# Performance work log

Measured on AMD Instinct MI355X. Metric: run time of the kernel, lower is better.

## Reference

```python
import jax, jax.numpy as jnp
import numpy as np

NBIT = 8


def _qmm(x, W, key):
    """Bit-serial quantized matmul with per-bit noisy weights (faithful to torch quantization()).
    x: (..., in), W: (out, in). Returns z (..., out), min, max, last noisy weight."""
    nsplit = 2 ** NBIT - 1
    mn = jnp.min(x)
    mx = jnp.max(x)
    q = ((x - mn) / (mx - mn) * nsplit).astype(jnp.uint8)  # trunc cast like torch .type(uint8)
    z = jnp.zeros(x.shape[:-1] + (W.shape[0],), x.dtype)
    Wn = W
    for i in range(NBIT):  # fixed 8-bit loop
        noise = jax.random.normal(jax.random.fold_in(key, i), W.shape, W.dtype) * jnp.abs(W) * 0.1
        Wn = W + noise
        bit = ((q >> i) & 1).astype(x.dtype) * float(2 ** i)
        z = z + jnp.matmul(bit, Wn.T)
    return z, mn, mx, Wn  # Wn = weight left in fc after loop (last bit's noisy weight)


def _requant(z, mn, mx, W_last):
    nsplit = 2 ** NBIT - 1
    bias = jnp.sum(mn * W_last, axis=1)  # (out,)
    return z / nsplit * (mx - mn) + bias


def _bn(x2d, gamma, beta, eps=1e-5):
    m = x2d.mean(axis=0)
    v = x2d.var(axis=0)  # biased, like torch BN training normalization
    return (x2d - m) / jnp.sqrt(v + eps) * gamma + beta


def _forward(node_embedding, edge_embedding, nbr_mask, c_two, c_two2, c_three, c_three2,
             bn2_g, bn2_b, bn3_g, bn3_b, nbr_idx):
    B, At, Nbr, Fe = edge_embedding.shape
    Fn = node_embedding.shape[-1]
    gather = jax.vmap(lambda x, i: x[i])  # batched fancy gather along atom axis
    key = jax.random.key(42)

    # two-body
    node_i = jnp.broadcast_to(node_embedding[:, :, None, :], (B, At, Nbr, Fn))
    node_j = gather(node_embedding, nbr_idx) * nbr_mask[..., None]  # (B,At,Nbr,Fn)
    c2 = jnp.concatenate([node_i, node_j], axis=3)  # (B,At,Nbr,2Fn)
    z, mn, mx, Wl = _qmm(c2, c_two, jax.random.fold_in(key, 0))
    c2 = jax.nn.relu(_requant(z, mn, mx, Wl))
    z, mn, mx, Wl = _qmm(c2, c_two2, jax.random.fold_in(key, 1))
    c2 = _requant(z, mn, mx, Wl)
    g2, e2 = jnp.split(c2, 2, axis=3)
    two = jax.nn.sigmoid(g2) * jnp.tanh(e2)
    two = _bn(two.reshape(-1, Fe), bn2_g, bn2_b).reshape(B, At, Nbr, Fe)

    # three-body
    nbr_jk = gather(nbr_idx, nbr_idx)                 # (B,At,Nbr,Nbr) neighbors-of-neighbors
    node_k = gather(node_embedding, nbr_jk)           # (B,At,Nbr,Nbr,Fn)
    edge_jk = gather(edge_embedding, nbr_idx)         # (B,At,Nbr,Nbr,Fe)
    edge_ij = jnp.broadcast_to(edge_embedding[:, :, :, None, :], (B, At, Nbr, Nbr, Fe))
    c3 = jnp.concatenate([
        jnp.broadcast_to(node_i[:, :, :, None, :], (B, At, Nbr, Nbr, Fn)),
        jnp.broadcast_to(node_j[:, :, :, None, :], (B, At, Nbr, Nbr, Fn)),
        node_k, edge_ij, edge_jk], axis=4)            # (B,At,Nbr,Nbr,3Fn+2Fe)
    z, mn, mx, Wl = _qmm(c3, c_three, jax.random.fold_in(key, 2))
    c3 = jax.nn.relu(_requant(z, mn, mx, Wl))
    z, mn, mx, Wl = _qmm(c3, c_three2, jax.random.fold_in(key, 3))
    c3 = _requant(z, mn, mx, Wl)
    g3, e3 = jnp.split(c3, 2, axis=4)
    three = jax.nn.sigmoid(g3) * jnp.tanh(e3)
    mask_jk = gather(nbr_mask, nbr_idx)               # (B,At,Nbr,Nbr) = nbr_mask[b, nbr_idx[b,i,j], k]
    three = (three * mask_jk[..., None]).sum(axis=3)  # (B,At,Nbr,Fe)
    three = _bn(three.reshape(-1, Fe), bn3_g, bn3_b).reshape(B, At, Nbr, Fe)

    return jax.nn.relu(edge_embedding + two + three)


def setup_inputs() -> dict:
    key = jax.random.key(0)
    ks = jax.random.split(key, 8)
    B, At, Nbr, Fn, Fe = 4, 48, 20, 64, 64
    return {
        "node_embedding": jax.random.normal(ks[0], (B, At, Fn), jnp.float32),
        "edge_embedding": jax.random.normal(ks[1], (B, At, Nbr, Fe), jnp.float32),
        "nbr_mask": jnp.ones((B, At, Nbr), jnp.float32),
        "c_two": jax.random.normal(ks[2], (8 * Fn, 2 * Fn), jnp.float32) * 0.05,
        "c_two2": jax.random.normal(ks[3], (2 * Fe, 8 * Fn), jnp.float32) * 0.05,
        "c_three": jax.random.normal(ks[4], (6 * Fn + 4 * Fe, 3 * Fn + 2 * Fe), jnp.float32) * 0.05,
        "c_three2": jax.random.normal(ks[5], (2 * Fe, 6 * Fn + 4 * Fe), jnp.float32) * 0.05,
        "bn2_g": jnp.ones((Fe,), jnp.float32),
        "bn2_b": jnp.zeros((Fe,), jnp.float32),
        "bn3_g": jnp.ones((Fe,), jnp.float32),
        "bn3_b": jnp.zeros((Fe,), jnp.float32),
        "nbr_idx": jax.random.randint(ks[6], (B, At, Nbr), 0, At, jnp.int32),
    }


def reference(node_embedding, edge_embedding, nbr_mask, c_two, c_two2, c_three, c_three2,
              bn2_g, bn2_b, bn3_g, bn3_b, nbr_idx):
    return _forward(node_embedding, edge_embedding, nbr_mask, c_two, c_two2, c_three, c_three2,
                    bn2_g, bn2_b, bn3_g, bn3_b, nbr_idx)
```

## Files before the change

kernel.cpp:

```cpp
#include <hip/hip_runtime.h>
#include <cstdint>
#include <cstddef>

#define DEVI __device__ __forceinline__

typedef __attribute__((ext_vector_type(8))) short s8v;
typedef __attribute__((ext_vector_type(4))) float f4v;

static constexpr int B_ = 4, AT = 48, NBRS = 20;
static constexpr int R2 = B_ * AT * NBRS;
static constexpr int M4 = R2 * NBRS;

static constexpr size_t OFF_B2A  = 0;
static constexpr size_t OFF_B2B  = OFF_B2A + 524288;
static constexpr size_t OFF_B3A  = OFF_B2B + 524288;
static constexpr size_t OFF_BW3B = OFF_B3A + 1638400;
static constexpr size_t OFF_BN3B = OFF_BW3B + 81920;
static constexpr size_t OFF_W72A = OFF_BN3B + 327680;
static constexpr size_t OFF_W72B = OFF_W72A + 65536;
static constexpr size_t OFF_W73A = OFF_W72B + 65536;
static constexpr size_t OFF_W73B = OFF_W73A + 204800;
static constexpr size_t OFF_RS   = OFF_W73B + 81920;
static constexpr size_t OFF_SLOT = OFF_RS + 1408;
static constexpr size_t OFF_BN   = OFF_SLOT + 16;
static constexpr size_t OFF_C2IN = OFF_BN + 256;
static constexpr size_t OFF_Z1   = OFF_C2IN + (size_t)R2 * 128;
static constexpr size_t OFF_C2B  = OFF_Z1 + (size_t)R2 * 512;
static constexpr size_t OFF_Z2   = OFF_C2B + (size_t)R2 * 512;
static constexpr size_t OFF_TWO  = OFF_Z2 + (size_t)R2 * 128;
static constexpr size_t OFF_NK   = OFF_TWO + (size_t)R2 * 64;
static constexpr size_t OFF_P2   = OFF_NK + (size_t)R2 * 64;
static constexpr size_t OFF_P3   = OFF_P2 + (size_t)R2 * 640;
static constexpr size_t OFF_TSUM = OFF_P3 + (size_t)R2 * 640;
static constexpr size_t OFF_Q2A  = OFF_TSUM + (size_t)R2 * 64;
static constexpr size_t OFF_Q2B  = OFF_Q2A + 122880;
static constexpr size_t OFF_QP2  = OFF_Q2B + 491520;
static constexpr size_t OFF_QP3  = OFF_QP2 + 184320;

DEVI void tf2x32(unsigned k0, unsigned k1, unsigned x0, unsigned x1,
                 unsigned& o0, unsigned& o1) {
  unsigned ks0 = k0, ks1 = k1, ks2 = k0 ^ k1 ^ 0x1BD11BDAu;
  x0 += ks0; x1 += ks1;
  const unsigned rotA[4] = {13u, 15u, 26u, 6u};
  const unsigned rotB[4] = {17u, 29u, 16u, 24u};
  unsigned ks[3] = {ks0, ks1, ks2};
  #pragma unroll
  for (int i = 0; i < 5; ++i) {
    const unsigned* rot = (i & 1) ? rotB : rotA;
    #pragma unroll
    for (int r = 0; r < 4; ++r) {
      x0 += x1;
      x1 = (x1 << rot[r]) | (x1 >> (32u - rot[r]));
      x1 ^= x0;
    }
    x0 += ks[(i + 1) % 3];
    x1 += ks[(i + 2) % 3] + (unsigned)(i + 1);
  }
  o0 = x0; o1 = x1;
}

DEVI float erfinv_xla(float x) {
  float w = -log1pf(-x * x);
  float p;
  if (w < 5.f) {
    w -= 2.5f;
    p = 2.81022636e-08f;
    p = fmaf(p, w, 3.43273939e-07f);
    p = fmaf(p, w, -3.5233877e-06f);
    p = fmaf(p, w, -4.39150654e-06f);
    p = fmaf(p, w, 0.00021858087f);
    p = fmaf(p, w, -0.00125372503f);
    p = fmaf(p, w, -0.00417768164f);
    p = fmaf(p, w, 0.246640727f);
    p = fmaf(p, w, 1.50140941f);
  } else {
    w = sqrtf(w) - 3.f;
    p = -0.000200214257f;
    p = fmaf(p, w, 0.000100950558f);
    p = fmaf(p, w, 0.00134934322f);
    p = fmaf(p, w, -0.00367342844f);
    p = fmaf(p, w, 0.00573950773f);
    p = fmaf(p, w, -0.0076224613f);
    p = fmaf(p, w, 0.00943887047f);
    p = fmaf(p, w, 1.00167406f);
    p = fmaf(p, w, 2.83297682f);
  }
  return p * x;
}

DEVI float normal_from_bits(unsigned bits) {
  unsigned fb = (bits >> 9) | 0x3F800000u;
  float f = __uint_as_float(fb) - 1.0f;
  const float lo = -0.99999994f;
  float u = f * (1.0f - lo) + lo;
  u = fmaxf(lo, u);
  return 1.41421356237f * erfinv_xla(u);
}

DEVI unsigned f2o(float f) { unsigned u = __float_as_uint(f); return (u & 0x80000000u) ? ~u : (u | 0x80000000u); }
DEVI float o2f(unsigned u) { return (u & 0x80000000u) ? __uint_as_float(u & 0x7FFFFFFFu) : __uint_as_float(~u); }

DEVI unsigned short f2bf(float x) {
  unsigned u = __float_as_uint(x);
  return (unsigned short)((u + 0x7FFFu + ((u >> 16) & 1u)) >> 16);
}
DEVI float bf2f(unsigned short h) { return __uint_as_float((unsigned)h << 16); }

DEVI void blockMinMax(float lmn, float lmx, float* smem, unsigned* slot) {
  float* smn = smem; float* smx = smem + 256;
  int t = threadIdx.x;
  smn[t] = lmn; smx[t] = lmx;
  __syncthreads();
  for (int s = 128; s > 0; s >>= 1) {
    if (t < s) { smn[t] = fminf(smn[t], smn[t + s]); smx[t] = fmaxf(smx[t], smx[t + s]); }
    __syncthreads();
  }
  if (t == 0) { atomicMin(slot + 0, f2o(smn[0])); atomicMax(slot + 1, f2o(smx[0])); }
}

DEVI s8v expand_mul(unsigned b) {
  unsigned sl = (b & 15u) * 0x00204081u;
  unsigned sh = ((b >> 4) & 15u) * 0x00204081u;
  union { unsigned u[4]; s8v s; } r;
  r.u[0] = (sl & 0x00010001u) * 0x3F80u;
  r.u[1] = ((sl >> 8) & 0x00010001u) * 0x3F80u;
  r.u[2] = (sh & 0x00010001u) * 0x3F80u;
  r.u[3] = ((sh >> 8) & 0x00010001u) * 0x3F80u;
  return r.s;
}
DEVI int bperm(int bit) { return bit ^ ((((bit) ^ (bit >> 1)) & 1) * 3); }

DEVI s8v bytes_to_bf16(unsigned a, unsigned b) {
  union { unsigned u[4]; s8v s; } r;
  float f0 = (float)(a & 255u), f1 = (float)((a >> 8) & 255u);
  float f2 = (float)((a >> 16) & 255u), f3 = (float)(a >> 24);
  r.u[0] = (__float_as_uint(f0) >> 16) | (__float_as_uint(f1) & 0xFFFF0000u);
  r.u[1] = (__float_as_uint(f2) >> 16) | (__float_as_uint(f3) & 0xFFFF0000u);
  f0 = (float)(b & 255u); f1 = (float)((b >> 8) & 255u);
  f2 = (float)((b >> 16) & 255u); f3 = (float)(b >> 24);
  r.u[2] = (__float_as_uint(f0) >> 16) | (__float_as_uint(f1) & 0xFFFF0000u);
  r.u[3] = (__float_as_uint(f2) >> 16) | (__float_as_uint(f3) & 0xFFFF0000u);
  return r.s;
}

__global__ __launch_bounds__(256) void k_prep(
    const float* __restrict__ W2A, const float* __restrict__ W2B,
    const float* __restrict__ W3A, const float* __restrict__ W3B,
    short* __restrict__ B2A, short* __restrict__ B2B, short* __restrict__ B3A,
    short* __restrict__ BW3B, short* __restrict__ BN3B,
    float* __restrict__ W72A, float* __restrict__ W72B,
    float* __restrict__ W73A, float* __restrict__ W73B,
    float* __restrict__ z1, float* __restrict__ z2, float* __restrict__ tsum,
    unsigned* __restrict__ slots) {
  int t = blockIdx.x * 256 + threadIdx.x;
  if (t < R2 * 512) z1[t] = 0.f;
  if (t < R2 * 128) z2[t] = 0.f;
  if (t < R2 * 64) tsum[t] = 0.f;
  if (t < 4) { slots[2 * t] = f2o(3.402823466e38f); slots[2 * t + 1] = f2o(-3.402823466e38f); }
  int lt = t;
  const float* W; float* W7; int N, K; unsigned layer; int which;
  if (lt < 524288) { W = W2A; W7 = W72A; N = 512; K = 128; layer = 0u; which = 0; }
  else if ((lt -= 524288) < 524288) { W = W2B; W7 = W72B; N = 128; K = 512; layer = 1u; which = 1; }
  else if ((lt -= 524288) < 1638400) { W = W3A; W7 = W73A; N = 640; K = 320; layer = 2u; which = 2; }
  else if ((lt -= 1638400) < 655360) { W = W3B; W7 = W73B; N = 128; K = 640; layer = 3u; which = 3; }
  else return;
  int n_elem = N * K;
  int bit = lt / n_elem;
  int e = lt - bit * n_elem;
  unsigned kl0, kl1, kb0, kb1, r0, r1;
  tf2x32(0u, 42u, 0u, layer, kl0, kl1);
  tf2x32(kl0, kl1, 0u, (unsigned)bit, kb0, kb1);
  tf2x32(kb0, kb1, 0u, (unsigned)e, r0, r1);
  float w = W[e];
  float nz = normal_from_bits(r0 ^ r1) * fabsf(w) * 0.1f;
  float wn = w + nz;
  int n = e / K, k = e - n * K;
  if (bit == 7) W7[e] = wn;
  if (which == 3) {
    BN3B[((size_t)(n >> 4) * 160 + (size_t)(k >> 2)) * 512
         + (size_t)((k & 3) * 16 + (n & 15)) * 8 + bperm(bit)] = (short)f2bf(ldexpf(nz, bit));
    if (bit == 0) {
      unsigned short hi = f2bf(w);
      unsigned short lo = f2bf(w - bf2f(hi));
      size_t o2 = (((size_t)(n >> 4) * 20 + (size_t)(k >> 5)) * 2) * 512
                + (size_t)(((k >> 3) & 3) * 16 + (n & 15)) * 8 + (k & 7);
      BW3B[o2] = (short)hi; BW3B[o2 + 512] = (short)lo;
    }
  } else {
    float sv = ldexpf(wn, bit);
    unsigned short hi = f2bf(sv);
    unsigned short lo = f2bf(sv - bf2f(hi));
    int pk = k;
    if (which == 2) {
      if (k >= 128 && k < 192) pk = k + 64;
      else if (k >= 192 && k < 256) pk = k - 64;
    }
    short* Bf = (which == 0) ? B2A : (which == 1 ? B2B : B3A);
    int KG = K >> 2;
    size_t off = (((size_t)(n >> 4) * KG + (size_t)(pk >> 2)) * 2) * 512
               + (size_t)((pk & 3) * 16 + (n & 15)) * 8 + bperm(bit);
    Bf[off] = (short)hi; Bf[off + 512] = (short)lo;
  }
}

__global__ __launch_bounds__(256) void k_build2(
    const float* __restrict__ node, const float* __restrict__ mask,
    const int* __restrict__ nidx, float* __restrict__ c2in, float* __restrict__ NK,
    const float* __restrict__ W72A, const float* __restrict__ W72B,
    const float* __restrict__ W73A, const float* __restrict__ W73B,
    float* __restrict__ rs, unsigned* __restrict__ slot) {
  __shared__ float sred[512];
  int idx = blockIdx.x * 256 + threadIdx.x;
  float lmn = 3.4e38f, lmx = -3.4e38f;
  if (idx < R2 * 128) {
    int row = idx >> 7, c = idx & 127;
    float v;
    if (c < 64) v = node[(size_t)(row / 20) * 64 + c];
    else {
      int b = row / 960;
      v = node[(size_t)(b * 48 + nidx[row]) * 64 + (c - 64)] * mask[row];
    }
    c2in[idx] = v; lmn = v; lmx = v;
  } else if (idx < R2 * 192) {
    int i2 = idx - R2 * 128;
    int row = i2 >> 6, c = i2 & 63;
    int b = row / 960;
    NK[i2] = node[(size_t)(b * 48 + nidx[row]) * 64 + c];
  } else if (idx < R2 * 192 + 1408) {
    int o = idx - R2 * 192;
    const float* p; int cols; int dsto;
    if (o < 512) { p = W72A; cols = 128; dsto = o; }
    else if (o < 640) { p = W72B; cols = 512; dsto = o; o -= 512; }
    else if (o < 1280) { p = W73A; cols = 320; dsto = o; o -= 640; }
    else { p = W73B; cols = 640; dsto = o; o -= 1280; }
    const float* rowp = p + (size_t)o * cols;
    float s = 0.f;
    for (int j = 0; j < cols; ++j) s += rowp[j];
    rs[dsto] = s;
  }
  blockMinMax(lmn, lmx, sred, slot);
}

__global__ __launch_bounds__(256) void k_qm4(
    const float* __restrict__ node, const float* __restrict__ edge,
    const float* __restrict__ c2in, const float* __restrict__ NK,
    const int* __restrict__ nidx, const unsigned* __restrict__ slot0,
    unsigned char* __restrict__ Q2A, unsigned* __restrict__ slot4) {
  __shared__ float sred[512];
  int idx0 = blockIdx.x * 256 + threadIdx.x;
  if (idx0 < R2 * 128) {
    const float mn = o2f(slot0[0]), mx = o2f(slot0[1]);
    float invd = 255.f / (mx - mn);
    Q2A[idx0] = (unsigned char)((c2in[idx0] - mn) * invd);
  }
  const int n0 = 12288, n1 = n0 + 245760, n2 = n1 + 245760, total = n2 + 4915200;
  float lmn = 3.4e38f, lmx = -3.4e38f;
  for (int idx = idx0; idx < total; idx += gridDim.x * 256) {
    float v, v2;
    if (idx < n0) { v = node[idx]; v2 = v; }
    else if (idx < n1) { v = edge[idx - n0]; v2 = v; }
    else if (idx < n2) {
      int j = idx - n1; int r = j >> 6, c = j & 63;
      v = c2in[(size_t)r * 128 + 64 + c]; v2 = v;
    } else {
      int j = idx - n2; int bij = j / 1280, t = j - bij * 1280;
      int b = bij / 960;
      size_t base = (size_t)((b * 48 + nidx[bij]) * 20) * 64 + t;
      v = NK[base]; v2 = edge[base];
    }
    lmn = fminf(lmn, fminf(v, v2)); lmx = fmaxf(lmx, fmaxf(v, v2));
  }
  blockMinMax(lmn, lmx, sred, slot4);
}

__global__ __launch_bounds__(256) void k_mfma_gemm(
    const unsigned char* __restrict__ Q, int ldq,
    const short* __restrict__ B, int KGfull, int kg0,
    int M, int Nfull, int KB, float* __restrict__ Z, int accflag) {
  const int tid = threadIdx.x;
  const int lane = tid & 63, w = tid >> 6;
  const int l15 = lane & 15, l4 = lane >> 4;
  const int mbase = blockIdx.y * 64;
  const int nbase = blockIdx.x * 128;
  const int kq0 = blockIdx.z * KB;
  f4v acc[4][2];
  #pragma unroll
  for (int a = 0; a < 4; ++a)
    #pragma unroll
    for (int b = 0; b < 2; ++b) acc[a][b] = f4v{0.f, 0.f, 0.f, 0.f};
  for (int ks16 = 0; ks16 < KB; ks16 += 16) {
    uint4 qv[4];
    #pragma unroll
    for (int mf = 0; mf < 4; ++mf)
      qv[mf] = *(const uint4*)(Q + (size_t)(mbase + mf * 16 + l15) * ldq + kq0 + ks16);
    #pragma unroll
    for (int sub = 0; sub < 4; ++sub) {
      int kg = kg0 + ((kq0 + ks16) >> 2) + sub;
      s8v af[4];
      #pragma unroll
      for (int mf = 0; mf < 4; ++mf) {
        unsigned wv = (sub == 0) ? qv[mf].x : (sub == 1) ? qv[mf].y : (sub == 2) ? qv[mf].z : qv[mf].w;
        af[mf] = expand_mul((wv >> (l4 * 8)) & 255u);
      }
      #pragma unroll
      for (int j = 0; j < 2; ++j) {
        size_t o = (((size_t)(nbase / 16 + w * 2 + j) * KGfull + kg) * 2) * 512 + (size_t)lane * 8;
        s8v bh = *(const s8v*)(B + o);
        s8v bl = *(const s8v*)(B + o + 512);
        #pragma unroll
        for (int mf = 0; mf < 4; ++mf) {
          acc[mf][j] = __builtin_amdgcn_mfma_f32_16x16x32_bf16(af[mf], bh, acc[mf][j], 0, 0, 0);
          acc[mf][j] = __builtin_amdgcn_mfma_f32_16x16x32_bf16(af[mf], bl, acc[mf][j], 0, 0, 0);
        }
      }
    }
  }
  #pragma unroll
  for (int mf = 0; mf < 4; ++mf) {
    #pragma unroll
    for (int r = 0; r < 4; ++r) {
      int m = mbase + mf * 16 + l4 * 4 + r;
      float* zp = Z + (size_t)m * Nfull + nbase;
      #pragma unroll
      for (int j = 0; j < 2; ++j) {
        int n = (w * 2 + j) * 16 + l15;
        if (accflag == 0) zp[n] = acc[mf][j][r];
        else atomicAdd(zp + n, acc[mf][j][r]);
      }
    }
  }
}

__global__ __launch_bounds__(256) void k_act1(const float* __restrict__ z1, const float* __restrict__ rs,
                                              const unsigned* __restrict__ slot0,
                                              unsigned* __restrict__ slot1) {
  __shared__ float sred[512];
  const float mn = o2f(slot0[0]), mx = o2f(slot0[1]);
  int idx = blockIdx.x * 256 + threadIdx.x;
  float lmn = 3.4e38f, lmx = -3.4e38f;
  if (idx < R2 * 512) {
    int o = idx & 511;
    float v = fmaxf(0.f, z1[idx] * (1.f / 255.f) * (mx - mn) + mn * rs[o]);
    lmn = v; lmx = v;
  }
  blockMinMax(lmn, lmx, sred, slot1);
}

__global__ __launch_bounds__(256) void k_qq(
    const float* __restrict__ z1, const float* __restrict__ rs,
    const float* __restrict__ node, const float* __restrict__ edge,
    const float* __restrict__ c2in, const float* __restrict__ NK,
    const int* __restrict__ nidx, const unsigned* __restrict__ slot0,
    const unsigned* __restrict__ slot2, const unsigned* __restrict__ slot4,
    unsigned char* __restrict__ Q2B, unsigned char* __restrict__ QP2, unsigned char* __restrict__ QP3) {
  int idx = blockIdx.x * 256 + threadIdx.x;
  if (idx < R2 * 512) {
    const float mn0 = o2f(slot0[0]), mx0 = o2f(slot0[1]);
    const float mn = o2f(slot2[0]), mx = o2f(slot2[1]);
    int o = idx & 511;
    float v = fmaxf(0.f, z1[idx] * (1.f / 255.f) * (mx0 - mn0) + mn0 * rs[o]);
    Q2B[idx] = (unsigned char)((v - mn) * (255.f / (mx - mn)));
    return;
  }
  int j = idx - R2 * 512;
  const int seg = 245760;
  if (j >= 5 * seg) return;
  const float mn = o2f(slot4[0]), mx = o2f(slot4[1]);
  const float invd = 255.f / (mx - mn);
  int s = j / seg; int jj = j - s * seg;
  int r = jj >> 6, c = jj & 63;
  float v; unsigned char* dst;
  if (s == 0)      { v = node[(size_t)(r / 20) * 64 + c];  dst = QP2 + (size_t)r * 192 + c; }
  else if (s == 1) { v = c2in[(size_t)r * 128 + 64 + c];   dst = QP2 + (size_t)r * 192 + 64 + c; }
  else if (s == 2) { v = edge[(size_t)r * 64 + c];         dst = QP2 + (size_t)r * 192 + 128 + c; }
  else if (s == 3) { v = NK[(size_t)r * 64 + c];           dst = QP3 + (size_t)r * 128 + c; }
  else             { v = edge[(size_t)r * 64 + c];         dst = QP3 + (size_t)r * 128 + 64 + c; }
  *dst = (unsigned char)((v - mn) * invd);
}

__global__ __launch_bounds__(256) void k_mfma_p23(
    const unsigned char* __restrict__ Q2, const unsigned char* __restrict__ Q3,
    const short* __restrict__ B, float* __restrict__ P2, float* __restrict__ P3) {
  const int half = blockIdx.y >= 60;
  const int by = blockIdx.y - half * 60;
  const unsigned char* Q = half ? Q3 : Q2;
  float* Z = half ? P3 : P2;
  const int kg0 = half ? 48 : 0;
  const int KB = half ? 128 : 192;
  const int ldq = half ? 128 : 192;
  const int tid = threadIdx.x;
  const int lane = tid & 63, w = tid >> 6;
  const int l15 = lane & 15, l4 = lane >> 4;
  const int mbase = by * 64;
  const int nbase = blockIdx.x * 128;
  f4v acc[4][2];
  #pragma unroll
  for (int a = 0; a < 4; ++a)
    #pragma unroll
    for (int b = 0; b < 2; ++b) acc[a][b] = f4v{0.f, 0.f, 0.f, 0.f};
  for (int ks16 = 0; ks16 < KB; ks16 += 16) {
    uint4 qv[4];
    #pragma unroll
    for (int mf = 0; mf < 4; ++mf)
      qv[mf] = *(const uint4*)(Q + (size_t)(mbase + mf * 16 + l15) * ldq + ks16);
    #pragma unroll
    for (int sub = 0; sub < 4; ++sub) {
      int kg = kg0 + (ks16 >> 2) + sub;
      s8v af[4];
      #pragma unroll
      for (int mf = 0; mf < 4; ++mf) {
        unsigned wv = (sub == 0) ? qv[mf].x : (sub == 1) ? qv[mf].y : (sub == 2) ? qv[mf].z : qv[mf].w;
        af[mf] = expand_mul((wv >> (l4 * 8)) & 255u);
      }
      #pragma unroll
      for (int j = 0; j < 2; ++j) {
        size_t o = (((size_t)(nbase / 16 + w * 2 + j) * 80 + kg) * 2) * 512 + (size_t)lane * 8;
        s8v bh = *(const s8v*)(B + o);
        s8v bl = *(const s8v*)(B + o + 512);
        #pragma unroll
        for (int mf = 0; mf < 4; ++mf) {
          acc[mf][j] = __builtin_amdgcn_mfma_f32_16x16x32_bf16(af[mf], bh, acc[mf][j], 0, 0, 0);
          acc[mf][j] = __builtin_amdgcn_mfma_f32_16x16x32_bf16(af[mf], bl, acc[mf][j], 0, 0, 0);
        }
      }
    }
  }
  #pragma unroll
  for (int mf = 0; mf < 4; ++mf) {
    #pragma unroll
    for (int r = 0; r < 4; ++r) {
      int m = mbase + mf * 16 + l4 * 4 + r;
      float* zp = Z + (size_t)m * 640 + nbase;
      #pragma unroll
      for (int j = 0; j < 2; ++j)
        zp[(w * 2 + j) * 16 + l15] = acc[mf][j][r];
    }
  }
}

__global__ __launch_bounds__(256) void k_act2mm3(
    const float* __restrict__ z2, const float* __restrict__ rs2b,
    const unsigned* __restrict__ slot2, float* __restrict__ two,
    const float* __restrict__ P12, const float* __restrict__ P3,
    const float* __restrict__ rs3a, const int* __restrict__ nidx,
    const unsigned* __restrict__ slot4, unsigned* __restrict__ slot6) {
  __shared__ float p12s[640];
  __shared__ float bias[640];
  __shared__ float sred[512];
  int gid = blockIdx.x * 256 + threadIdx.x;
  if (gid < R2 * 64) {
    const float mn = o2f(slot2[0]), mx = o2f(slot2[1]);
    int row = gid >> 6, c = gid & 63;
    float d = (mx - mn) * (1.f / 255.f);
    float g = z2[(size_t)row * 128 + c] * d + mn * rs2b[c];
    float e = z2[(size_t)row * 128 + 64 + c] * d + mn * rs2b[64 + c];
    two[gid] = (1.f / (1.f + expf(-g))) * tanhf(e);
  }
  const int bij = blockIdx.x;
  const int b = bij / 960;
  const int jp = nidx[bij];
  const size_t p3b = (size_t)((b * 48 + jp) * 20) * 640;
  const float mn2 = o2f(slot4[0]), mx2 = o2f(slot4[1]);
  const float sc2 = (mx2 - mn2) * (1.f / 255.f);
  for (int k = threadIdx.x; k < 640; k += 256) {
    p12s[k] = P12[(size_t)bij * 640 + k];
    bias[k] = mn2 * rs3a[k];
  }
  __syncthreads();
  float lmn = 3.4e38f, lmx = -3.4e38f;
  for (int t = threadIdx.x; t < 20 * 640; t += 256) {
    int knb = t / 640, k = t - knb * 640;
    float v = fmaxf(0.f, (p12s[k] + P3[p3b + t]) * sc2 + bias[k]);
    lmn = fminf(lmn, v); lmx = fmaxf(lmx, v);
  }
  blockMinMax(lmn, lmx, sred, slot6);
}

__global__ __launch_bounds__(256) void k_mfma_l3b(
    const float* __restrict__ P12, const float* __restrict__ P3,
    const float* __restrict__ rs3a, const float* __restrict__ rs3b,
    const short* __restrict__ BW, const short* __restrict__ BN,
    const int* __restrict__ nidx, const float* __restrict__ mask,
    const unsigned* __restrict__ slotA, const unsigned* __restrict__ slotB,
    float* __restrict__ tsum) {
  __shared__ unsigned char qt[64 * 648];
  const int tid = threadIdx.x;
  const int s0 = blockIdx.x * 64;
  const float mn2 = o2f(slotA[0]), mx2 = o2f(slotA[1]);
  const float mn3 = o2f(slotB[0]), mx3 = o2f(slotB[1]);
  const float sc2 = (mx2 - mn2) * (1.f / 255.f);
  const float invd3 = 255.f / (mx3 - mn3);
  {
    int r = tid >> 2, kq = (tid & 3) * 160;
    int s = s0 + r;
    int bij = s / 20, knb = s - bij * 20, b = bij / 960;
    int p3row = (b * 48 + nidx[bij]) * 20 + knb;
    const float* pa = P12 + (size_t)bij * 640;
    const float* pb = P3 + (size_t)p3row * 640;
    for (int k = kq; k < kq + 160; k += 4) {
      float4 va = *(const float4*)(pa + k);
      float4 vb = *(const float4*)(pb + k);
      float4 rv = *(const float4*)(rs3a + k);
      float v0 = fmaxf(0.f, (va.x + vb.x) * sc2 + mn2 * rv.x);
      float v1 = fmaxf(0.f, (va.y + vb.y) * sc2 + mn2 * rv.y);
      float v2 = fmaxf(0.f, (va.z + vb.z) * sc2 + mn2 * rv.z);
      float v3 = fmaxf(0.f, (va.w + vb.w) * sc2 + mn2 * rv.w);
      unsigned pk = (unsigned)((v0 - mn3) * invd3) | ((unsigned)((v1 - mn3) * invd3) << 8)
                  | ((unsigned)((v2 - mn3) * invd3) << 16) | ((unsigned)((v3 - mn3) * invd3) << 24);
      *(unsigned*)(&qt[(size_t)r * 648 + k]) = pk;
    }
  }
  __syncthreads();
  const int lane = tid & 63, w = tid >> 6;
  const int l15 = lane & 15, l4 = lane >> 4;
  const int nf0 = w, nf1 = w + 4;
  const unsigned char* qr[4];
  #pragma unroll
  for (int mf = 0; mf < 4; ++mf) qr[mf] = qt + (size_t)(mf * 16 + l15) * 648;
  const size_t bb0 = (size_t)nf0 * 160 * 512 + (size_t)lane * 8;
  const size_t bb1 = (size_t)nf1 * 160 * 512 + (size_t)lane * 8;
  f4v acc[4][2];
  #pragma unroll
  for (int a = 0; a < 4; ++a)
    #pragma unroll
    for (int b = 0; b < 2; ++b) acc[a][b] = f4v{0.f, 0.f, 0.f, 0.f};
  s8v c00 = *(const s8v*)(BN + bb0), c01 = *(const s8v*)(BN + bb1);
  s8v c10 = *(const s8v*)(BN + bb0 + 512), c11 = *(const s8v*)(BN + bb1 + 512);
  for (int c = 0; c < 20; ++c) {
    s8v bwh0 = *(const s8v*)(BW + (((size_t)nf0 * 20 + c) * 2) * 512 + (size_t)lane * 8);
    s8v bwh1 = *(const s8v*)(BW + (((size_t)nf1 * 20 + c) * 2) * 512 + (size_t)lane * 8);
    #pragma unroll
    for (int s = 0; s < 8; ++s) {
      const int kg = c * 8 + s;
      s8v af[4];
      #pragma unroll
      for (int mf = 0; mf < 4; ++mf) {
        unsigned wv = *(const unsigned*)(qr[mf] + kg * 4);
        af[mf] = expand_mul((wv >> (l4 * 8)) & 255u);
      }
      s8v nx0 = *(const s8v*)(BN + bb0 + (size_t)(kg + 2) * 512);
      s8v nx1 = *(const s8v*)(BN + bb1 + (size_t)(kg + 2) * 512);
      #pragma unroll
      for (int mf = 0; mf < 4; ++mf) {
        acc[mf][0] = __builtin_amdgcn_mfma_f32_16x16x32_bf16(af[mf], c00, acc[mf][0], 0, 0, 0);
        acc[mf][1] = __builtin_amdgcn_mfma_f32_16x16x32_bf16(af[mf], c01, acc[mf][1], 0, 0, 0);
      }
      c00 = c10; c01 = c11; c10 = nx0; c11 = nx1;
    }
    {
      s8v aq[4];
      #pragma unroll
      for (int mf = 0; mf < 4; ++mf) {
        unsigned a0 = *(const unsigned*)(qr[mf] + c * 32 + l4 * 8);
        unsigned a1 = *(const unsigned*)(qr[mf] + c * 32 + l4 * 8 + 4);
        aq[mf] = bytes_to_bf16(a0, a1);
      }
      #pragma unroll
      for (int mf = 0; mf < 4; ++mf) {
        acc[mf][0] = __builtin_amdgcn_mfma_f32_16x16x32_bf16(aq[mf], bwh0, acc[mf][0], 0, 0, 0);
        acc[mf][1] = __builtin_amdgcn_mfma_f32_16x16x32_bf16(aq[mf], bwh1, acc[mf][1], 0, 0, 0);
      }
      s8v bwl0 = *(const s8v*)(BW + ((((size_t)nf0 * 20 + c) * 2) + 1) * 512 + (size_t)lane * 8);
      s8v bwl1 = *(const s8v*)(BW + ((((size_t)nf1 * 20 + c) * 2) + 1) * 512 + (size_t)lane * 8);
      #pragma unroll
      for (int mf = 0; mf < 4; ++mf) {
        acc[mf][0] = __builtin_amdgcn_mfma_f32_16x16x32_bf16(aq[mf], bwl0, acc[mf][0], 0, 0, 0);
        acc[mf][1] = __builtin_amdgcn_mfma_f32_16x16x32_bf16(aq[mf], bwl1, acc[mf][1], 0, 0, 0);
      }
    }
  }
  const float d3 = (mx3 - mn3) * (1.f / 255.f);
  const int col = w * 16 + l15;
  const float rg = mn3 * rs3b[col];
  const float re = mn3 * rs3b[64 + col];
  #pragma unroll
  for (int mf = 0; mf < 4; ++mf) {
    #pragma unroll
    for (int r = 0; r < 4; ++r) {
      int s = s0 + mf * 16 + l4 * 4 + r;
      int bij = s / 20, knb = s - bij * 20, b = bij / 960;
      int p3row = (b * 48 + nidx[bij]) * 20 + knb;
      float mk = mask[p3row];
      float g = acc[mf][0][r] * d3 + rg;
      float e = acc[mf][1][r] * d3 + re;
      float val = (1.f / (1.f + expf(-g))) * tanhf(e) * mk;
      atomicAdd(&tsum[(size_t)bij * 64 + col], val);
    }
  }
}

__global__ __launch_bounds__(256) void k_bnstats2(const float* __restrict__ two, const float* __restrict__ tsum,
                                                  float* __restrict__ bn) {
  __shared__ float ss[512];
  const float* x = blockIdx.y ? tsum : two;
  float* mout = bn + (blockIdx.y ? 128 : 0);
  float* vout = mout + 64;
  int c = blockIdx.x, t = threadIdx.x;
  float s = 0.f, q = 0.f;
  for (int r = t; r < R2; r += 256) { float v = x[(size_t)r * 64 + c]; s += v; q += v * v; }
  ss[t] = s; ss[256 + t] = q;
  __syncthreads();
  for (int st = 128; st > 0; st >>= 1) {
    if (t < st) { ss[t] += ss[t + st]; ss[256 + t] += ss[256 + t + st]; }
    __syncthreads();
  }
  if (t == 0) { float m = ss[0] / (float)R2; mout[c] = m; vout[c] = ss[256] / (float)R2 - m * m; }
}

__global__ __launch_bounds__(256) void k_final(const float* __restrict__ edge, const float* __restrict__ two,
                                               const float* __restrict__ tsum, const float* __restrict__ bn,
                                               const float* __restrict__ g2, const float* __restrict__ b2,
                                               const float* __restrict__ g3, const float* __restrict__ b3,
                                               float* __restrict__ out) {
  int idx = blockIdx.x * 256 + threadIdx.x;
  if (idx >= R2 * 64) return;
  int c = idx & 63;
  float t2 = (two[idx] - bn[c]) / sqrtf(bn[64 + c] + 1e-5f) * g2[c] + b2[c];
  float t3 = (tsum[idx] - bn[128 + c]) / sqrtf(bn[192 + c] + 1e-5f) * g3[c] + b3[c];
  out[idx] = fmaxf(0.f, edge[idx] + t2 + t3);
}

extern "C" void kernel_launch(void* const* d_in, const int* in_sizes, int n_in,
                              void* d_out, int out_size, void* d_ws, size_t ws_size,
                              hipStream_t stream) {
  (void)in_sizes; (void)n_in; (void)out_size; (void)ws_size;
  const float* node   = (const float*)d_in[0];
  const float* edge   = (const float*)d_in[1];
  const float* mask   = (const float*)d_in[2];
  const float* c_two  = (const float*)d_in[3];
  const float* c_two2 = (const float*)d_in[4];
  const float* c_three  = (const float*)d_in[5];
  const float* c_three2 = (const float*)d_in[6];
  const float* bn2g = (const float*)d_in[7];
  const float* bn2b = (const float*)d_in[8];
  const float* bn3g = (const float*)d_in[9];
  const float* bn3b = (const float*)d_in[10];
  const int*   nidx = (const int*)d_in[11];
  float* ws = (float*)d_ws;
  unsigned* slots = (unsigned*)(ws + OFF_SLOT);
  float* out = (float*)d_out;
  short* B2A  = (short*)(ws + OFF_B2A);
  short* B2B  = (short*)(ws + OFF_B2B);
  short* B3A  = (short*)(ws + OFF_B3A);
  short* BW3B = (short*)(ws + OFF_BW3B);
  short* BN3B = (short*)(ws + OFF_BN3B);
  unsigned char* Q2A = (unsigned char*)(ws + OFF_Q2A);
  unsigned char* Q2B = (unsigned char*)(ws + OFF_Q2B);
  unsigned char* QP2 = (unsigned char*)(ws + OFF_QP2);
  unsigned char* QP3 = (unsigned char*)(ws + OFF_QP3);
  float* RS = ws + OFF_RS;

  k_prep<<<13056, 256, 0, stream>>>(c_two, c_two2, c_three, c_three2,
                                    B2A, B2B, B3A, BW3B, BN3B,
                                    ws + OFF_W72A, ws + OFF_W72B, ws + OFF_W73A, ws + OFF_W73B,
                                    ws + OFF_Z1, ws + OFF_Z2, ws + OFF_TSUM, slots);
  k_build2<<<2886, 256, 0, stream>>>(node, mask, nidx, ws + OFF_C2IN, ws + OFF_NK,
                                     ws + OFF_W72A, ws + OFF_W72B, ws + OFF_W73A, ws + OFF_W73B,
                                     RS, slots + 0);
  k_qm4<<<2048, 256, 0, stream>>>(node, edge, ws + OFF_C2IN, ws + OFF_NK, nidx, slots + 0,
                                  Q2A, slots + 4);
  k_mfma_gemm<<<dim3(4, 60, 2), 256, 0, stream>>>(Q2A, 128, B2A, 32, 0, 3840, 512, 64, ws + OFF_Z1, 3);
  k_act1<<<7680, 256, 0, stream>>>(ws + OFF_Z1, RS, slots + 0, slots + 2);
  k_qq<<<12480, 256, 0, stream>>>(ws + OFF_Z1, RS, node, edge, ws + OFF_C2IN, ws + OFF_NK,
                                  nidx, slots + 0, slots + 2, slots + 4, Q2B, QP2, QP3);
  k_mfma_gemm<<<dim3(1, 60, 4), 256, 0, stream>>>(Q2B, 512, B2B, 128, 0, 3840, 128, 128, ws + OFF_Z2, 3);
  k_mfma_p23<<<dim3(5, 120), 256, 0, stream>>>(QP2, QP3, B3A, ws + OFF_P2, ws + OFF_P3);
  k_act2mm3<<<3840, 256, 0, stream>>>(ws + OFF_Z2, RS + 512, slots + 2, ws + OFF_TWO,
                                      ws + OFF_P2, ws + OFF_P3, RS + 640, nidx, slots + 4, slots + 6);
  k_mfma_l3b<<<1200, 256, 0, stream>>>(ws + OFF_P2, ws + OFF_P3, RS + 640, RS + 1280,
                                       BW3B, BN3B, nidx, mask, slots + 4, slots + 6, ws + OFF_TSUM);
  k_bnstats2<<<dim3(64, 2), 256, 0, stream>>>(ws + OFF_TWO, ws + OFF_TSUM, ws + OFF_BN);
  k_final<<<960, 256, 0, stream>>>(edge, ws + OFF_TWO, ws + OFF_TSUM, ws + OFF_BN,
                                   bn2g, bn2b, bn3g, bn3b, out);
}
```

Measured before the change: 832.9 us.

## Split K across waves in l3b MFMA kernel with LDS cross-wave reduction

```diff
diff --git a/kernel.cpp b/kernel.cpp
--- a/kernel.cpp
+++ b/kernel.cpp
@@ -476,7 +476,7 @@
   blockMinMax(lmn, lmx, sred, slot6);
 }
 
-__global__ __launch_bounds__(256) void k_mfma_l3b(
+__global__ __launch_bounds__(256, 2) void k_mfma_l3b(
     const float* __restrict__ P12, const float* __restrict__ P3,
     const float* __restrict__ rs3a, const float* __restrict__ rs3b,
     const short* __restrict__ BW, const short* __restrict__ BN,
@@ -513,78 +513,88 @@
   __syncthreads();
   const int lane = tid & 63, w = tid >> 6;
   const int l15 = lane & 15, l4 = lane >> 4;
-  const int nf0 = w, nf1 = w + 4;
   const unsigned char* qr[4];
   #pragma unroll
   for (int mf = 0; mf < 4; ++mf) qr[mf] = qt + (size_t)(mf * 16 + l15) * 648;
-  const size_t bb0 = (size_t)nf0 * 160 * 512 + (size_t)lane * 8;
-  const size_t bb1 = (size_t)nf1 * 160 * 512 + (size_t)lane * 8;
-  f4v acc[4][2];
+  f4v acc[4][8];
   #pragma unroll
   for (int a = 0; a < 4; ++a)
     #pragma unroll
-    for (int b = 0; b < 2; ++b) acc[a][b] = f4v{0.f, 0.f, 0.f, 0.f};
-  s8v c00 = *(const s8v*)(BN + bb0), c01 = *(const s8v*)(BN + bb1);
-  s8v c10 = *(const s8v*)(BN + bb0 + 512), c11 = *(const s8v*)(BN + bb1 + 512);
-  for (int c = 0; c < 20; ++c) {
-    s8v bwh0 = *(const s8v*)(BW + (((size_t)nf0 * 20 + c) * 2) * 512 + (size_t)lane * 8);
-    s8v bwh1 = *(const s8v*)(BW + (((size_t)nf1 * 20 + c) * 2) * 512 + (size_t)lane * 8);
-    #pragma unroll
-    for (int s = 0; s < 8; ++s) {
-      const int kg = c * 8 + s;
-      s8v af[4];
+    for (int b = 0; b < 8; ++b) acc[a][b] = f4v{0.f, 0.f, 0.f, 0.f};
+  const int kg0 = w * 40;
+  s8v cur[8];
+  #pragma unroll
+  for (int j = 0; j < 8; ++j)
+    cur[j] = *(const s8v*)(BN + ((size_t)j * 160 + kg0) * 512 + (size_t)lane * 8);
+  for (int kgl = 0; kgl < 40; ++kgl) {
+    const int kg = kg0 + kgl;
+    s8v af[4];
+    #pragma unroll
+    for (int mf = 0; mf < 4; ++mf) {
+      unsigned wv = *(const unsigned*)(qr[mf] + kg * 4);
+      af[mf] = expand_mul((wv >> (l4 * 8)) & 255u);
+    }
+    s8v nxt[8];
+    #pragma unroll
+    for (int j = 0; j < 8; ++j)
+      nxt[j] = *(const s8v*)(BN + ((size_t)j * 160 + kg + 1) * 512 + (size_t)lane * 8);
+    #pragma unroll
+    for (int j = 0; j < 8; ++j) {
+      #pragma unroll
+      for (int mf = 0; mf < 4; ++mf)
+        acc[mf][j] = __builtin_amdgcn_mfma_f32_16x16x32_bf16(af[mf], cur[j], acc[mf][j], 0, 0, 0);
+    }
+    #pragma unroll
+    for (int j = 0; j < 8; ++j) cur[j] = nxt[j];
+  }
+  #pragma unroll
+  for (int cl = 0; cl < 5; ++cl) {
+    const int c = w * 5 + cl;
+    s8v aq[4];
+    #pragma unroll
+    for (int mf = 0; mf < 4; ++mf) {
+      unsigned a0 = *(const unsigned*)(qr[mf] + c * 32 + l4 * 8);
+      unsigned a1 = *(const unsigned*)(qr[mf] + c * 32 + l4 * 8 + 4);
+      aq[mf] = bytes_to_bf16(a0, a1);
+    }
+    #pragma unroll
+    for (int j = 0; j < 8; ++j) {
+      s8v bh = *(const s8v*)(BW + (((size_t)j * 20 + c) * 2) * 512 + (size_t)lane * 8);
+      s8v bl = *(const s8v*)(BW + (((size_t)j * 20 + c) * 2 + 1) * 512 + (size_t)lane * 8);
       #pragma unroll
       for (int mf = 0; mf < 4; ++mf) {
-        unsigned wv = *(const unsigned*)(qr[mf] + kg * 4);
-        af[mf] = expand_mul((wv >> (l4 * 8)) & 255u);
+        acc[mf][j] = __builtin_amdgcn_mfma_f32_16x16x32_bf16(aq[mf], bh, acc[mf][j], 0, 0, 0);
+        acc[mf][j] = __builtin_amdgcn_mfma_f32_16x16x32_bf16(aq[mf], bl, acc[mf][j], 0, 0, 0);
       }
-      s8v nx0 = *(const s8v*)(BN + bb0 + (size_t)(kg + 2) * 512);
-      s8v nx1 = *(const s8v*)(BN + bb1 + (size_t)(kg + 2) * 512);
-      #pragma unroll
-      for (int mf = 0; mf < 4; ++mf) {
-        acc[mf][0] = __builtin_amdgcn_mfma_f32_16x16x32_bf16(af[mf], c00, acc[mf][0], 0, 0, 0);
-        acc[mf][1] = __builtin_amdgcn_mfma_f32_16x16x32_bf16(af[mf], c01, acc[mf][1], 0, 0, 0);
-      }
-      c00 = c10; c01 = c11; c10 = nx0; c11 = nx1;
-    }
-    {
-      s8v aq[4];
-      #pragma unroll
-      for (int mf = 0; mf < 4; ++mf) {
-        unsigned a0 = *(const unsigned*)(qr[mf] + c * 32 + l4 * 8);
-        unsigned a1 = *(const unsigned*)(qr[mf] + c * 32 + l4 * 8 + 4);
-        aq[mf] = bytes_to_bf16(a0, a1);
-      }
-      #pragma unroll
-      for (int mf = 0; mf < 4; ++mf) {
-        acc[mf][0] = __builtin_amdgcn_mfma_f32_16x16x32_bf16(aq[mf], bwh0, acc[mf][0], 0, 0, 0);
-        acc[mf][1] = __builtin_amdgcn_mfma_f32_16x16x32_bf16(aq[mf], bwh1, acc[mf][1], 0, 0, 0);
-      }
-      s8v bwl0 = *(const s8v*)(BW + ((((size_t)nf0 * 20 + c) * 2) + 1) * 512 + (size_t)lane * 8);
-      s8v bwl1 = *(const s8v*)(BW + ((((size_t)nf1 * 20 + c) * 2) + 1) * 512 + (size_t)lane * 8);
-      #pragma unroll
-      for (int mf = 0; mf < 4; ++mf) {
-        acc[mf][0] = __builtin_amdgcn_mfma_f32_16x16x32_bf16(aq[mf], bwl0, acc[mf][0], 0, 0, 0);
-        acc[mf][1] = __builtin_amdgcn_mfma_f32_16x16x32_bf16(aq[mf], bwl1, acc[mf][1], 0, 0, 0);
-      }
-    }
-  }
+    }
+  }
+  float* zz = (float*)qt;
   const float d3 = (mx3 - mn3) * (1.f / 255.f);
-  const int col = w * 16 + l15;
-  const float rg = mn3 * rs3b[col];
-  const float re = mn3 * rs3b[64 + col];
-  #pragma unroll
   for (int mf = 0; mf < 4; ++mf) {
-    #pragma unroll
-    for (int r = 0; r < 4; ++r) {
-      int s = s0 + mf * 16 + l4 * 4 + r;
+    __syncthreads();
+    #pragma unroll
+    for (int j = 0; j < 8; ++j) {
+      #pragma unroll
+      for (int r = 0; r < 4; ++r)
+        zz[((size_t)w * 16 + l4 * 4 + r) * 132 + j * 16 + l15] = acc[mf][j][r];
+    }
+    __syncthreads();
+    #pragma unroll
+    for (int k = 0; k < 4; ++k) {
+      int o = tid + k * 256;
+      int row = o >> 6, cc = o & 63;
+      float zg = zz[(size_t)row * 132 + cc] + zz[(size_t)(16 + row) * 132 + cc]
+               + zz[(size_t)(32 + row) * 132 + cc] + zz[(size_t)(48 + row) * 132 + cc];
+      float ze = zz[(size_t)row * 132 + 64 + cc] + zz[(size_t)(16 + row) * 132 + 64 + cc]
+               + zz[(size_t)(32 + row) * 132 + 64 + cc] + zz[(size_t)(48 + row) * 132 + 64 + cc];
+      int s = s0 + mf * 16 + row;
       int bij = s / 20, knb = s - bij * 20, b = bij / 960;
       int p3row = (b * 48 + nidx[bij]) * 20 + knb;
       float mk = mask[p3row];
-      float g = acc[mf][0][r] * d3 + rg;
-      float e = acc[mf][1][r] * d3 + re;
+      float g = zg * d3 + mn3 * rs3b[cc];
+      float e = ze * d3 + mn3 * rs3b[64 + cc];
       float val = (1.f / (1.f + expf(-g))) * tanhf(e) * mk;
-      atomicAdd(&tsum[(size_t)bij * 64 + col], val);
+      atomicAdd(&tsum[(size_t)bij * 64 + cc], val);
     }
   }
 }
```

New measurement: 915.7 us. +9.9%, slower.

## Loop bits per thread in weight prep; retile l3b waves to 2x2 fragment grid

Applied to the files above, without the earlier changes.

```diff
diff --git a/kernel.cpp b/kernel.cpp
--- a/kernel.cpp
+++ b/kernel.cpp
@@ -128,7 +128,7 @@
   r.u[3] = ((sh >> 8) & 0x00010001u) * 0x3F80u;
   return r.s;
 }
-DEVI int bperm(int bit) { return bit ^ ((((bit) ^ (bit >> 1)) & 1) * 3); }
+DEVI constexpr int bperm(int bit) { return bit ^ ((((bit) ^ (bit >> 1)) & 1) * 3); }
 
 DEVI s8v bytes_to_bf16(unsigned a, unsigned b) {
   union { unsigned u[4]; s8v s; } r;
@@ -159,37 +159,45 @@
   if (t < 4) { slots[2 * t] = f2o(3.402823466e38f); slots[2 * t + 1] = f2o(-3.402823466e38f); }
   int lt = t;
   const float* W; float* W7; int N, K; unsigned layer; int which;
-  if (lt < 524288) { W = W2A; W7 = W72A; N = 512; K = 128; layer = 0u; which = 0; }
-  else if ((lt -= 524288) < 524288) { W = W2B; W7 = W72B; N = 128; K = 512; layer = 1u; which = 1; }
-  else if ((lt -= 524288) < 1638400) { W = W3A; W7 = W73A; N = 640; K = 320; layer = 2u; which = 2; }
-  else if ((lt -= 1638400) < 655360) { W = W3B; W7 = W73B; N = 128; K = 640; layer = 3u; which = 3; }
+  if (lt < 65536) { W = W2A; W7 = W72A; N = 512; K = 128; layer = 0u; which = 0; }
+  else if ((lt -= 65536) < 65536) { W = W2B; W7 = W72B; N = 128; K = 512; layer = 1u; which = 1; }
+  else if ((lt -= 65536) < 204800) { W = W3A; W7 = W73A; N = 640; K = 320; layer = 2u; which = 2; }
+  else if ((lt -= 204800) < 81920) { W = W3B; W7 = W73B; N = 128; K = 640; layer = 3u; which = 3; }
   else return;
-  int n_elem = N * K;
-  int bit = lt / n_elem;
-  int e = lt - bit * n_elem;
-  unsigned kl0, kl1, kb0, kb1, r0, r1;
+  int e = lt;
+  int n = e / K, k = e - n * K;
+  float w = W[e];
+  float aw = fabsf(w) * 0.1f;
+  unsigned kl0, kl1;
   tf2x32(0u, 42u, 0u, layer, kl0, kl1);
-  tf2x32(kl0, kl1, 0u, (unsigned)bit, kb0, kb1);
-  tf2x32(kb0, kb1, 0u, (unsigned)e, r0, r1);
-  float w = W[e];
-  float nz = normal_from_bits(r0 ^ r1) * fabsf(w) * 0.1f;
-  float wn = w + nz;
-  int n = e / K, k = e - n * K;
-  if (bit == 7) W7[e] = wn;
+  union { short s[8]; s8v v; } hv, lv, bnv;
+  #pragma unroll
+  for (int bit = 0; bit < 8; ++bit) {
+    unsigned kb0, kb1, r0, r1;
+    tf2x32(kl0, kl1, 0u, (unsigned)bit, kb0, kb1);
+    tf2x32(kb0, kb1, 0u, (unsigned)e, r0, r1);
+    float nz = normal_from_bits(r0 ^ r1) * aw;
+    float wn = w + nz;
+    if (bit == 7) W7[e] = wn;
+    if (which == 3) {
+      bnv.s[bperm(bit)] = (short)f2bf(ldexpf(nz, bit));
+    } else {
+      float sv = ldexpf(wn, bit);
+      unsigned short hi = f2bf(sv);
+      unsigned short lo = f2bf(sv - bf2f(hi));
+      hv.s[bperm(bit)] = (short)hi;
+      lv.s[bperm(bit)] = (short)lo;
+    }
+  }
   if (which == 3) {
-    BN3B[((size_t)(n >> 4) * 160 + (size_t)(k >> 2)) * 512
-         + (size_t)((k & 3) * 16 + (n & 15)) * 8 + bperm(bit)] = (short)f2bf(ldexpf(nz, bit));
-    if (bit == 0) {
-      unsigned short hi = f2bf(w);
-      unsigned short lo = f2bf(w - bf2f(hi));
-      size_t o2 = (((size_t)(n >> 4) * 20 + (size_t)(k >> 5)) * 2) * 512
-                + (size_t)(((k >> 3) & 3) * 16 + (n & 15)) * 8 + (k & 7);
-      BW3B[o2] = (short)hi; BW3B[o2 + 512] = (short)lo;
-    }
+    *(s8v*)(BN3B + ((size_t)(n >> 4) * 160 + (size_t)(k >> 2)) * 512
+                 + (size_t)((k & 3) * 16 + (n & 15)) * 8) = bnv.v;
+    unsigned short hi = f2bf(w);
+    unsigned short lo = f2bf(w - bf2f(hi));
+    size_t o2 = (((size_t)(n >> 4) * 20 + (size_t)(k >> 5)) * 2) * 512
+              + (size_t)(((k >> 3) & 3) * 16 + (n & 15)) * 8 + (k & 7);
+    BW3B[o2] = (short)hi; BW3B[o2 + 512] = (short)lo;
   } else {
-    float sv = ldexpf(wn, bit);
-    unsigned short hi = f2bf(sv);
-    unsigned short lo = f2bf(sv - bf2f(hi));
     int pk = k;
     if (which == 2) {
       if (k >= 128 && k < 192) pk = k + 64;
@@ -198,8 +206,9 @@
     short* Bf = (which == 0) ? B2A : (which == 1 ? B2B : B3A);
     int KG = K >> 2;
     size_t off = (((size_t)(n >> 4) * KG + (size_t)(pk >> 2)) * 2) * 512
-               + (size_t)((pk & 3) * 16 + (n & 15)) * 8 + bperm(bit);
-    Bf[off] = (short)hi; Bf[off + 512] = (short)lo;
+               + (size_t)((pk & 3) * 16 + (n & 15)) * 8;
+    *(s8v*)(Bf + off) = hv.v;
+    *(s8v*)(Bf + off + 512) = lv.v;
   }
 }
 
@@ -511,80 +520,95 @@
     }
   }
   __syncthreads();
-  const int lane = tid & 63, w = tid >> 6;
+  const int lane = tid & 63, wave = tid >> 6;
+  const int wm = wave >> 1, wn = wave & 1;
   const int l15 = lane & 15, l4 = lane >> 4;
-  const int nf0 = w, nf1 = w + 4;
-  const unsigned char* qr[4];
-  #pragma unroll
-  for (int mf = 0; mf < 4; ++mf) qr[mf] = qt + (size_t)(mf * 16 + l15) * 648;
-  const size_t bb0 = (size_t)nf0 * 160 * 512 + (size_t)lane * 8;
-  const size_t bb1 = (size_t)nf1 * 160 * 512 + (size_t)lane * 8;
-  f4v acc[4][2];
-  #pragma unroll
-  for (int a = 0; a < 4; ++a)
-    #pragma unroll
-    for (int b = 0; b < 2; ++b) acc[a][b] = f4v{0.f, 0.f, 0.f, 0.f};
-  s8v c00 = *(const s8v*)(BN + bb0), c01 = *(const s8v*)(BN + bb1);
-  s8v c10 = *(const s8v*)(BN + bb0 + 512), c11 = *(const s8v*)(BN + bb1 + 512);
+  const int nfl[4] = {2 * wn, 2 * wn + 1, 2 * wn + 4, 2 * wn + 5};
+  size_t bb[4];
+  #pragma unroll
+  for (int j = 0; j < 4; ++j) bb[j] = ((size_t)nfl[j] * 160) * 512 + (size_t)lane * 8;
+  f4v acc[2][4];
+  #pragma unroll
+  for (int a = 0; a < 2; ++a)
+    #pragma unroll
+    for (int b = 0; b < 4; ++b) acc[a][b] = f4v{0.f, 0.f, 0.f, 0.f};
+  s8v c0[4], c1[4];
+  #pragma unroll
+  for (int j = 0; j < 4; ++j) {
+    c0[j] = *(const s8v*)(BN + bb[j]);
+    c1[j] = *(const s8v*)(BN + bb[j] + 512);
+  }
+  const unsigned char* qrow0 = &qt[(size_t)(wm * 32 + l15) * 648];
+  const unsigned char* qrow1 = qrow0 + 16 * 648;
   for (int c = 0; c < 20; ++c) {
-    s8v bwh0 = *(const s8v*)(BW + (((size_t)nf0 * 20 + c) * 2) * 512 + (size_t)lane * 8);
-    s8v bwh1 = *(const s8v*)(BW + (((size_t)nf1 * 20 + c) * 2) * 512 + (size_t)lane * 8);
+    s8v bwh[4];
+    #pragma unroll
+    for (int j = 0; j < 4; ++j)
+      bwh[j] = *(const s8v*)(BW + (((size_t)nfl[j] * 20 + c) * 2) * 512 + (size_t)lane * 8);
     #pragma unroll
     for (int s = 0; s < 8; ++s) {
       const int kg = c * 8 + s;
-      s8v af[4];
-      #pragma unroll
-      for (int mf = 0; mf < 4; ++mf) {
-        unsigned wv = *(const unsigned*)(qr[mf] + kg * 4);
-        af[mf] = expand_mul((wv >> (l4 * 8)) & 255u);
-      }
-      s8v nx0 = *(const s8v*)(BN + bb0 + (size_t)(kg + 2) * 512);
-      s8v nx1 = *(const s8v*)(BN + bb1 + (size_t)(kg + 2) * 512);
-      #pragma unroll
-      for (int mf = 0; mf < 4; ++mf) {
-        acc[mf][0] = __builtin_amdgcn_mfma_f32_16x16x32_bf16(af[mf], c00, acc[mf][0], 0, 0, 0);
-        acc[mf][1] = __builtin_amdgcn_mfma_f32_16x16x32_bf16(af[mf], c01, acc[mf][1], 0, 0, 0);
-      }
-      c00 = c10; c01 = c11; c10 = nx0; c11 = nx1;
+      unsigned w0 = *(const unsigned*)(qrow0 + kg * 4);
+      unsigned w1 = *(const unsigned*)(qrow1 + kg * 4);
+      s8v af0 = expand_mul((w0 >> (l4 * 8)) & 255u);
+      s8v af1 = expand_mul((w1 >> (l4 * 8)) & 255u);
+      s8v nx[4];
+      #pragma unroll
+      for (int j = 0; j < 4; ++j)
+        nx[j] = *(const s8v*)(BN + bb[j] + (size_t)(kg + 2) * 512);
+      __builtin_amdgcn_s_setprio(1);
+      #pragma unroll
+      for (int j = 0; j < 4; ++j) {
+        acc[0][j] = __builtin_amdgcn_mfma_f32_16x16x32_bf16(af0, c0[j], acc[0][j], 0, 0, 0);
+        acc[1][j] = __builtin_amdgcn_mfma_f32_16x16x32_bf16(af1, c0[j], acc[1][j], 0, 0, 0);
+      }
+      __builtin_amdgcn_s_setprio(0);
+      #pragma unroll
+      for (int j = 0; j < 4; ++j) { c0[j] = c1[j]; c1[j] = nx[j]; }
     }
     {
-      s8v aq[4];
-      #pragma unroll
-      for (int mf = 0; mf < 4; ++mf) {
-        unsigned a0 = *(const unsigned*)(qr[mf] + c * 32 + l4 * 8);
-        unsigned a1 = *(const unsigned*)(qr[mf] + c * 32 + l4 * 8 + 4);
-        aq[mf] = bytes_to_bf16(a0, a1);
-      }
-      #pragma unroll
-      for (int mf = 0; mf < 4; ++mf) {
-        acc[mf][0] = __builtin_amdgcn_mfma_f32_16x16x32_bf16(aq[mf], bwh0, acc[mf][0], 0, 0, 0);
-        acc[mf][1] = __builtin_amdgcn_mfma_f32_16x16x32_bf16(aq[mf], bwh1, acc[mf][1], 0, 0, 0);
-      }
-      s8v bwl0 = *(const s8v*)(BW + ((((size_t)nf0 * 20 + c) * 2) + 1) * 512 + (size_t)lane * 8);
-      s8v bwl1 = *(const s8v*)(BW + ((((size_t)nf1 * 20 + c) * 2) + 1) * 512 + (size_t)lane * 8);
-      #pragma unroll
-      for (int mf = 0; mf < 4; ++mf) {
-        acc[mf][0] = __builtin_amdgcn_mfma_f32_16x16x32_bf16(aq[mf], bwl0, acc[mf][0], 0, 0, 0);
-        acc[mf][1] = __builtin_amdgcn_mfma_f32_16x16x32_bf16(aq[mf], bwl1, acc[mf][1], 0, 0, 0);
-      }
+      const int x = c * 32 + l4 * 8;
+      unsigned a0 = *(const unsigned*)(qrow0 + x);
+      unsigned a1 = *(const unsigned*)(qrow0 + x + 4);
+      s8v aq0 = bytes_to_bf16(a0, a1);
+      a0 = *(const unsigned*)(qrow1 + x);
+      a1 = *(const unsigned*)(qrow1 + x + 4);
+      s8v aq1 = bytes_to_bf16(a0, a1);
+      __builtin_amdgcn_s_setprio(1);
+      #pragma unroll
+      for (int j = 0; j < 4; ++j) {
+        acc[0][j] = __builtin_amdgcn_mfma_f32_16x16x32_bf16(aq0, bwh[j], acc[0][j], 0, 0, 0);
+        acc[1][j] = __builtin_amdgcn_mfma_f32_16x16x32_bf16(aq1, bwh[j], acc[1][j], 0, 0, 0);
+        s8v bwl = *(const s8v*)(BW + ((((size_t)nfl[j] * 20 + c) * 2) + 1) * 512 + (size_t)lane * 8);
+        acc[0][j] = __builtin_amdgcn_mfma_f32_16x16x32_bf16(aq0, bwl, acc[0][j], 0, 0, 0);
+        acc[1][j] = __builtin_amdgcn_mfma_f32_16x16x32_bf16(aq1, bwl, acc[1][j], 0, 0, 0);
+      }
+      __builtin_amdgcn_s_setprio(0);
     }
   }
   const float d3 = (mx3 - mn3) * (1.f / 255.f);
-  const int col = w * 16 + l15;
-  const float rg = mn3 * rs3b[col];
-  const float re = mn3 * rs3b[64 + col];
-  #pragma unroll
-  for (int mf = 0; mf < 4; ++mf) {
+  float rg[2], re[2];
+  #pragma unroll
+  for (int j = 0; j < 2; ++j) {
+    int gcol = (2 * wn + j) * 16 + l15;
+    rg[j] = mn3 * rs3b[gcol];
+    re[j] = mn3 * rs3b[64 + gcol];
+  }
+  #pragma unroll
+  for (int mf = 0; mf < 2; ++mf) {
     #pragma unroll
     for (int r = 0; r < 4; ++r) {
-      int s = s0 + mf * 16 + l4 * 4 + r;
+      int s = s0 + wm * 32 + mf * 16 + l4 * 4 + r;
       int bij = s / 20, knb = s - bij * 20, b = bij / 960;
       int p3row = (b * 48 + nidx[bij]) * 20 + knb;
       float mk = mask[p3row];
-      float g = acc[mf][0][r] * d3 + rg;
-      float e = acc[mf][1][r] * d3 + re;
-      float val = (1.f / (1.f + expf(-g))) * tanhf(e) * mk;
-      atomicAdd(&tsum[(size_t)bij * 64 + col], val);
+      #pragma unroll
+      for (int j = 0; j < 2; ++j) {
+        float g = acc[mf][j][r] * d3 + rg[j];
+        float e = acc[mf][j + 2][r] * d3 + re[j];
+        float val = (1.f / (1.f + expf(-g))) * tanhf(e) * mk;
+        atomicAdd(&tsum[(size_t)bij * 64 + (2 * wn + j) * 16 + l15], val);
+      }
     }
   }
 }
@@ -650,10 +674,10 @@
   unsigned char* QP3 = (unsigned char*)(ws + OFF_QP3);
   float* RS = ws + OFF_RS;
 
-  k_prep<<<13056, 256, 0, stream>>>(c_two, c_two2, c_three, c_three2,
-                                    B2A, B2B, B3A, BW3B, BN3B,
-                                    ws + OFF_W72A, ws + OFF_W72B, ws + OFF_W73A, ws + OFF_W73B,
-                                    ws + OFF_Z1, ws + OFF_Z2, ws + OFF_TSUM, slots);
+  k_prep<<<7680, 256, 0, stream>>>(c_two, c_two2, c_three, c_three2,
+                                   B2A, B2B, B3A, BW3B, BN3B,
+                                   ws + OFF_W72A, ws + OFF_W72B, ws + OFF_W73A, ws + OFF_W73B,
+                                   ws + OFF_Z1, ws + OFF_Z2, ws + OFF_TSUM, slots);
   k_build2<<<2886, 256, 0, stream>>>(node, mask, nidx, ws + OFF_C2IN, ws + OFF_NK,
                                      ws + OFF_W72A, ws + OFF_W72B, ws + OFF_W73A, ws + OFF_W73B,
                                      RS, slots + 0);
```

Measured after the change: 807.6 us. 1.03x faster.
